# Performance work log

Hardware: AMD Instinct MI355X
Metric: run time of the kernel (lower is better)

The kernel has to match this reference:

```python
import jax, jax.numpy as jnp
import numpy as np

TEMPERATURE = 1.0
NEG_INF = -1e30  # finite stand-in for -inf: safe for log_softmax and its vjp


def setup_inputs() -> dict:
    key = jax.random.key(0)
    k1, k2 = jax.random.split(key)
    B, M, D = 4096, 3, 256
    tokens = jax.random.normal(k1, (B, M, D), dtype=jnp.float32)
    labels = jax.random.randint(k2, (B,), 0, 32, dtype=jnp.int32)
    return {"tokens": tokens, "labels": labels}


def reference(tokens, labels):
    # tokens: [B, M, D]; labels: [B]
    B, M, D = tokens.shape
    # Pairwise per-modality similarities: sim[i, k, m] = <tokens[i,m], tokens[k,m]>
    sim = jnp.einsum('imd,kmd->ikm', tokens, tokens) / TEMPERATURE
    self_mask = jnp.eye(B, dtype=bool)
    # Original excludes sample i itself from the candidate set; masking with a
    # huge negative logit makes it contribute 0 to the softmax partition.
    sim = jnp.where(self_mask[:, :, None], NEG_INF, sim)
    logp = jax.nn.log_softmax(sim, axis=1)  # softmax over the B-1 other samples

    # Positive pairs: same label, excluding self.
    pos = (labels[:, None] == labels[None, :]) & ~self_mask  # [B, B]
    pos_count = pos.sum(axis=1)                               # [B]
    valid = pos_count > 0                                     # sum(same_label) > 1

    # Mean log-prob over positives, per (sample, modality).
    pos_logp = jnp.einsum('ikm,ik->im', logp, pos.astype(logp.dtype))  # [B, M]
    denom = jnp.maximum(pos_count, 1).astype(logp.dtype)[:, None]
    per = jnp.where(valid[:, None], pos_logp / denom, 0.0)             # [B, M]

    num = valid.sum() * M
    return -per.sum() / num.astype(per.dtype)
```

## Files before the change

### kernel.cpp

```cpp
#include <hip/hip_runtime.h>

#define B_N 4096
#define M_N 3
#define D_N 256
#define LOG2E 1.44269504088896340736f
#define LN2   0.69314718055994530942f
#define C_OFF   64.0f
#define T_CLAMP 112.0f

typedef __bf16 bf16x8 __attribute__((ext_vector_type(8)));
typedef float  f32x4  __attribute__((ext_vector_type(4)));

__device__ __forceinline__ unsigned short f2bf(float f) {
    unsigned int u = __float_as_uint(f);
    u += 0x7FFFu + ((u >> 16) & 1u);
    return (unsigned short)(u >> 16);
}
__device__ __forceinline__ float bf2f(unsigned short h) {
    return __uint_as_float(((unsigned int)h) << 16);
}

__global__ void cvt_kernel(const float* __restrict__ in, unsigned short* __restrict__ out,
                           float* __restrict__ norm2) {
    int idx = blockIdx.x * blockDim.x + threadIdx.x;
    float4 v = reinterpret_cast<const float4*>(in)[idx];
    int i   = idx / 192;
    int rem = idx - i * 192;
    int m   = rem >> 6;
    int d4  = rem & 63;
    ushort4 o;
    o.x = f2bf(v.x); o.y = f2bf(v.y); o.z = f2bf(v.z); o.w = f2bf(v.w);
    reinterpret_cast<ushort4*>(out)[((size_t)m * B_N + i) * 64 + d4] = o;
    float nx = bf2f(o.x), ny = bf2f(o.y), nz = bf2f(o.z), nw = bf2f(o.w);
    float s = nx * nx + ny * ny + nz * nz + nw * nw;
#pragma unroll
    for (int msk = 1; msk < 64; msk <<= 1) s += __shfl_xor(s, msk);
    if ((threadIdx.x & 63) == 0) norm2[m * B_N + i] = s;
}

__global__ __launch_bounds__(256, 3) void main_kernel(
    const unsigned short* __restrict__ tokb, const int* __restrict__ labels,
    float2* __restrict__ partials) {
    int raw = blockIdx.x;
    int bid = (raw & 7) * 96 + (raw >> 3);
    int m  = bid >> 8;
    int ns = (bid >> 5) & 7;
    int rb = bid & 31;
    int i0 = rb * 128;
    int cb = ns * 512;

    int tid  = threadIdx.x;
    int wave = tid >> 6, lane = tid & 63;
    int lr = lane & 15, lk = lane >> 4;
    const unsigned short* tm = tokb + (size_t)m * (B_N * D_N);

    __shared__ __align__(16) char ldsB[2][8192];
    __shared__ int labl[512];
    labl[tid]       = labels[cb + tid];
    labl[tid + 256] = labels[cb + tid + 256];

    int r0 = i0 + wave * 32;
    bf16x8 afrag[2][8];
#pragma unroll
    for (int rt = 0; rt < 2; ++rt) {
        const unsigned short* rp = tm + (size_t)(r0 + rt * 16 + lr) * D_N + lk * 8;
#pragma unroll
        for (int kf = 0; kf < 8; ++kf)
            afrag[rt][kf] = *reinterpret_cast<const bf16x8*>(rp + kf * 32);
    }
    int labr[2][4];
#pragma unroll
    for (int rt = 0; rt < 2; ++rt)
#pragma unroll
        for (int j = 0; j < 4; ++j)
            labr[rt][j] = labels[r0 + rt * 16 + lk * 4 + j];

    float S[2][4] = {{0.f, 0.f, 0.f, 0.f}, {0.f, 0.f, 0.f, 0.f}};
    float P[2][4] = {{0.f, 0.f, 0.f, 0.f}, {0.f, 0.f, 0.f, 0.f}};

    int lc  = tid >> 5;
    int w   = tid & 31;
    int sch = w ^ (lc & 7);
    const unsigned short* sbase = tm + (size_t)(cb + lc) * D_N + sch * 8;

    {
        bf16x8 t0 = *reinterpret_cast<const bf16x8*>(sbase);
        bf16x8 t1 = *reinterpret_cast<const bf16x8*>(sbase + 8 * D_N);
        *reinterpret_cast<bf16x8*>(&ldsB[0][tid * 16])        = t0;
        *reinterpret_cast<bf16x8*>(&ldsB[0][4096 + tid * 16]) = t1;
    }

    for (int kb = 0; kb < 32; ++kb) {
        int cur = kb & 1;
        __syncthreads();

        int nkb = (kb + 1) & 31;
        const unsigned short* np = sbase + (size_t)nkb * (16 * D_N);
        bf16x8 nt0 = *reinterpret_cast<const bf16x8*>(np);
        bf16x8 nt1 = *reinterpret_cast<const bf16x8*>(np + 8 * D_N);

        const char* bp = ldsB[cur];
        int swz = (lr & 7) << 4;
        bf16x8 bfrag[8];
#pragma unroll
        for (int kf = 0; kf < 8; ++kf)
            bfrag[kf] = *reinterpret_cast<const bf16x8*>(
                bp + lr * 512 + ((((kf * 4 + lk) << 4)) ^ swz));
        int labc = labl[kb * 16 + lr];

        f32x4 acc0 = {0.f, 0.f, 0.f, 0.f};
        f32x4 acc1 = {0.f, 0.f, 0.f, 0.f};
#pragma unroll
        for (int kf = 0; kf < 8; ++kf) {
            acc0 = __builtin_amdgcn_mfma_f32_16x16x32_bf16(afrag[0][kf], bfrag[kf], acc0, 0, 0, 0);
            acc1 = __builtin_amdgcn_mfma_f32_16x16x32_bf16(afrag[1][kf], bfrag[kf], acc1, 0, 0, 0);
        }

        int cg0 = cb + kb * 16;
        if ((cg0 < r0 + 32) && (cg0 + 16 > r0)) {
            int colg = cg0 + lr;
#pragma unroll
            for (int rt = 0; rt < 2; ++rt) {
                f32x4 aa = rt ? acc1 : acc0;
#pragma unroll
                for (int j = 0; j < 4; ++j) {
                    float s = aa[j];
                    float t = fminf(fmaf(s, LOG2E, -C_OFF), T_CLAMP);
                    float e = __builtin_amdgcn_exp2f(t);
                    int row = r0 + rt * 16 + lk * 4 + j;
                    e = (colg == row) ? 0.f : e;
                    S[rt][j] += e;
                    P[rt][j] += (labc == labr[rt][j]) ? s : 0.f;
                }
            }
        } else {
#pragma unroll
            for (int rt = 0; rt < 2; ++rt) {
                f32x4 aa = rt ? acc1 : acc0;
#pragma unroll
                for (int j = 0; j < 4; ++j) {
                    float s = aa[j];
                    float t = fminf(fmaf(s, LOG2E, -C_OFF), T_CLAMP);
                    S[rt][j] += __builtin_amdgcn_exp2f(t);
                    P[rt][j] += (labc == labr[rt][j]) ? s : 0.f;
                }
            }
        }

        char* dst = (char*)ldsB[cur ^ 1];
        *reinterpret_cast<bf16x8*>(dst + tid * 16)        = nt0;
        *reinterpret_cast<bf16x8*>(dst + 4096 + tid * 16) = nt1;
    }

#pragma unroll
    for (int rt = 0; rt < 2; ++rt)
#pragma unroll
        for (int j = 0; j < 4; ++j) {
            float sv = S[rt][j], pv = P[rt][j];
#pragma unroll
            for (int msk = 1; msk < 16; msk <<= 1) {
                sv += __shfl_xor(sv, msk);
                pv += __shfl_xor(pv, msk);
            }
            if (lr == 0) {
                int rl = rt * 16 + lk * 4 + j;
                float2 q; q.x = sv; q.y = pv;
                partials[(size_t)(((m * 32 + rb) * 8 + ns) * 128) + wave * 32 + rl] = q;
            }
        }
}

__global__ void reduce_kernel(const float2* __restrict__ partials,
                              const float* __restrict__ norm2,
                              const int* __restrict__ labels,
                              float* __restrict__ blockpart,
                              int* __restrict__ nvout) {
    __shared__ int h[32];
    int tid = threadIdx.x;
    if (tid < 32) h[tid] = 0;
    __syncthreads();
    for (int i = tid; i < B_N; i += 256) atomicAdd(&h[labels[i]], 1);
    __syncthreads();
    if (blockIdx.x == 0 && tid == 0) {
        int nv = 0;
#pragma unroll
        for (int c = 0; c < 32; ++c) nv += (h[c] >= 2) ? h[c] : 0;
        nvout[0] = nv;
    }
    int gid = blockIdx.x * 256 + tid;
    int m = gid >> 12, i = gid & 4095;
    int rb = i >> 7, r = i & 127;
    const float2* pp = partials + (size_t)(((m * 32 + rb) * 8) * 128) + r;
    float S = 0.f, P = 0.f;
#pragma unroll
    for (int ns = 0; ns < 8; ++ns) {
        float2 q = pp[ns * 128];
        S += q.x; P += q.y;
    }
    P -= norm2[gid];
    int pc = h[labels[i]] - 1;
    float contrib = (pc > 0)
        ? (__builtin_amdgcn_logf(S) + C_OFF) * LN2 - P / (float)pc
        : 0.f;
#pragma unroll
    for (int off = 32; off >= 1; off >>= 1) contrib += __shfl_down(contrib, off);
    __shared__ float w4[4];
    if ((tid & 63) == 0) w4[tid >> 6] = contrib;
    __syncthreads();
    if (tid == 0) blockpart[blockIdx.x] = w4[0] + w4[1] + w4[2] + w4[3];
}

__global__ void final_kernel(const float* __restrict__ blockpart, const int* __restrict__ nv,
                             float* __restrict__ out) {
    int lane = threadIdx.x;
    float s = (lane < 48) ? blockpart[lane] : 0.f;
#pragma unroll
    for (int off = 32; off >= 1; off >>= 1) s += __shfl_down(s, off);
    if (lane == 0) out[0] = s / (float)(nv[0] * M_N);
}

extern "C" void kernel_launch(void* const* d_in, const int* in_sizes, int n_in,
                              void* d_out, int out_size, void* d_ws, size_t ws_size,
                              hipStream_t stream) {
    const float* tokens = (const float*)d_in[0];
    const int*   labels = (const int*)d_in[1];
    float* out = (float*)d_out;

    char* ws = (char*)d_ws;
    int*    nv        = (int*)(ws + 128);
    float*  blockpart = (float*)(ws + 256);
    float*  norm2     = (float*)(ws + 1024);
    float2* partials  = (float2*)(ws + 65536);
    unsigned short* tokb = (unsigned short*)(ws + 1048576);

    cvt_kernel<<<3072, 256, 0, stream>>>(tokens, tokb, norm2);
    main_kernel<<<768, 256, 0, stream>>>(tokb, labels, partials);
    reduce_kernel<<<48, 256, 0, stream>>>(partials, norm2, labels, blockpart, nv);
    final_kernel<<<1, 64, 0, stream>>>(blockpart, nv, out);
}
```

Measured before the change: 51.25 us.

## Exploit Gram-matrix symmetry by computing only upper-triangular tiles with column sums

The similarity matrix is symmetric, so the main kernel now computes only the upper-triangular 256x256 tile pairs per modality: 136 instead of all pairs. Each off-diagonal tile adds its row-wise exp and positive sums to the row block and also writes column-wise sums, reduced across waves through shared memory, for the mirrored block. This is meant to roughly halve the MFMA and exp work. Per-tile partials are now stored as bf16 and reduced over 16 slots, and occupancy drops to 2 blocks per CU to make room for the larger register tiles. The bf16 partial sums lower the accuracy of the final loss.

```diff
diff --git a/kernel.cpp b/kernel.cpp
--- a/kernel.cpp
+++ b/kernel.cpp
@@ -38,16 +38,18 @@
     if ((threadIdx.x & 63) == 0) norm2[m * B_N + i] = s;
 }
 
-__global__ __launch_bounds__(256, 3) void main_kernel(
+__global__ __launch_bounds__(256, 2) void main_kernel(
     const unsigned short* __restrict__ tokb, const int* __restrict__ labels,
-    float2* __restrict__ partials) {
+    unsigned short* __restrict__ partials) {
     int raw = blockIdx.x;
-    int bid = (raw & 7) * 96 + (raw >> 3);
-    int m  = bid >> 8;
-    int ns = (bid >> 5) & 7;
-    int rb = bid & 31;
-    int i0 = rb * 128;
-    int cb = ns * 512;
+    int bid = (raw & 7) * 51 + (raw >> 3);
+    int m    = bid / 136;
+    int beta = bid - m * 136;
+    int b = 0;
+    while ((b + 1) * (b + 2) / 2 <= beta) ++b;
+    int a = beta - (b * (b + 1)) / 2;
+    bool offd = (a != b);
+    int cb = b * 256;
 
     int tid  = threadIdx.x;
     int wave = tid >> 6, lane = tid & 63;
@@ -55,28 +57,31 @@
     const unsigned short* tm = tokb + (size_t)m * (B_N * D_N);
 
     __shared__ __align__(16) char ldsB[2][8192];
-    __shared__ int labl[512];
-    labl[tid]       = labels[cb + tid];
-    labl[tid + 256] = labels[cb + tid + 256];
-
-    int r0 = i0 + wave * 32;
-    bf16x8 afrag[2][8];
-#pragma unroll
-    for (int rt = 0; rt < 2; ++rt) {
+    __shared__ int labl[256];
+    __shared__ float colbuf[4][16][16][2];
+    labl[tid] = labels[cb + tid];
+
+    int r0 = a * 256 + wave * 64;
+    bf16x8 afrag[4][8];
+#pragma unroll
+    for (int rt = 0; rt < 4; ++rt) {
         const unsigned short* rp = tm + (size_t)(r0 + rt * 16 + lr) * D_N + lk * 8;
 #pragma unroll
         for (int kf = 0; kf < 8; ++kf)
             afrag[rt][kf] = *reinterpret_cast<const bf16x8*>(rp + kf * 32);
     }
-    int labr[2][4];
-#pragma unroll
-    for (int rt = 0; rt < 2; ++rt)
+    int labr[4][4];
+#pragma unroll
+    for (int rt = 0; rt < 4; ++rt)
 #pragma unroll
         for (int j = 0; j < 4; ++j)
             labr[rt][j] = labels[r0 + rt * 16 + lk * 4 + j];
 
-    float S[2][4] = {{0.f, 0.f, 0.f, 0.f}, {0.f, 0.f, 0.f, 0.f}};
-    float P[2][4] = {{0.f, 0.f, 0.f, 0.f}, {0.f, 0.f, 0.f, 0.f}};
+    float S[4][4], P[4][4];
+#pragma unroll
+    for (int rt = 0; rt < 4; ++rt)
+#pragma unroll
+        for (int j = 0; j < 4; ++j) { S[rt][j] = 0.f; P[rt][j] = 0.f; }
 
     int lc  = tid >> 5;
     int w   = tid & 31;
@@ -90,11 +95,11 @@
         *reinterpret_cast<bf16x8*>(&ldsB[0][4096 + tid * 16]) = t1;
     }
 
-    for (int kb = 0; kb < 32; ++kb) {
+    for (int kb = 0; kb < 16; ++kb) {
         int cur = kb & 1;
         __syncthreads();
 
-        int nkb = (kb + 1) & 31;
+        int nkb = (kb + 1) & 15;
         const unsigned short* np = sbase + (size_t)nkb * (16 * D_N);
         bf16x8 nt0 = *reinterpret_cast<const bf16x8*>(np);
         bf16x8 nt1 = *reinterpret_cast<const bf16x8*>(np + 8 * D_N);
@@ -105,55 +110,66 @@
 #pragma unroll
         for (int kf = 0; kf < 8; ++kf)
             bfrag[kf] = *reinterpret_cast<const bf16x8*>(
-                bp + lr * 512 + ((((kf * 4 + lk) << 4)) ^ swz));
+                bp + lr * 512 + (((kf * 4 + lk) << 4) ^ swz));
         int labc = labl[kb * 16 + lr];
 
-        f32x4 acc0 = {0.f, 0.f, 0.f, 0.f};
-        f32x4 acc1 = {0.f, 0.f, 0.f, 0.f};
+        f32x4 acc[4];
+#pragma unroll
+        for (int rt = 0; rt < 4; ++rt) acc[rt] = f32x4{0.f, 0.f, 0.f, 0.f};
 #pragma unroll
         for (int kf = 0; kf < 8; ++kf) {
-            acc0 = __builtin_amdgcn_mfma_f32_16x16x32_bf16(afrag[0][kf], bfrag[kf], acc0, 0, 0, 0);
-            acc1 = __builtin_amdgcn_mfma_f32_16x16x32_bf16(afrag[1][kf], bfrag[kf], acc1, 0, 0, 0);
+#pragma unroll
+            for (int rt = 0; rt < 4; ++rt)
+                acc[rt] = __builtin_amdgcn_mfma_f32_16x16x32_bf16(
+                    afrag[rt][kf], bfrag[kf], acc[rt], 0, 0, 0);
         }
 
+        float cs = 0.f, cp = 0.f;
         int cg0 = cb + kb * 16;
-        if ((cg0 < r0 + 32) && (cg0 + 16 > r0)) {
+        if ((cg0 < r0 + 64) && (cg0 + 16 > r0)) {
             int colg = cg0 + lr;
 #pragma unroll
-            for (int rt = 0; rt < 2; ++rt) {
-                f32x4 aa = rt ? acc1 : acc0;
+            for (int rt = 0; rt < 4; ++rt) {
 #pragma unroll
                 for (int j = 0; j < 4; ++j) {
-                    float s = aa[j];
-                    float t = fminf(fmaf(s, LOG2E, -C_OFF), T_CLAMP);
+                    float s2 = acc[rt][j];
+                    float t = fminf(fmaf(s2, LOG2E, -C_OFF), T_CLAMP);
                     float e = __builtin_amdgcn_exp2f(t);
                     int row = r0 + rt * 16 + lk * 4 + j;
                     e = (colg == row) ? 0.f : e;
-                    S[rt][j] += e;
-                    P[rt][j] += (labc == labr[rt][j]) ? s : 0.f;
+                    bool mt = (labc == labr[rt][j]);
+                    S[rt][j] += e;  P[rt][j] += mt ? s2 : 0.f;
+                    cs += e;        cp += mt ? s2 : 0.f;
                 }
             }
         } else {
 #pragma unroll
-            for (int rt = 0; rt < 2; ++rt) {
-                f32x4 aa = rt ? acc1 : acc0;
+            for (int rt = 0; rt < 4; ++rt) {
 #pragma unroll
                 for (int j = 0; j < 4; ++j) {
-                    float s = aa[j];
-                    float t = fminf(fmaf(s, LOG2E, -C_OFF), T_CLAMP);
-                    S[rt][j] += __builtin_amdgcn_exp2f(t);
-                    P[rt][j] += (labc == labr[rt][j]) ? s : 0.f;
+                    float s2 = acc[rt][j];
+                    float t = fminf(fmaf(s2, LOG2E, -C_OFF), T_CLAMP);
+                    float e = __builtin_amdgcn_exp2f(t);
+                    bool mt = (labc == labr[rt][j]);
+                    S[rt][j] += e;  P[rt][j] += mt ? s2 : 0.f;
+                    cs += e;        cp += mt ? s2 : 0.f;
                 }
             }
         }
+
+        cs += __shfl_xor(cs, 16); cs += __shfl_xor(cs, 32);
+        cp += __shfl_xor(cp, 16); cp += __shfl_xor(cp, 32);
+        if (lk == 0) { colbuf[wave][kb][lr][0] = cs; colbuf[wave][kb][lr][1] = cp; }
 
         char* dst = (char*)ldsB[cur ^ 1];
         *reinterpret_cast<bf16x8*>(dst + tid * 16)        = nt0;
         *reinterpret_cast<bf16x8*>(dst + 4096 + tid * 16) = nt1;
     }
 
-#pragma unroll
-    for (int rt = 0; rt < 2; ++rt)
+    __syncthreads();
+
+#pragma unroll
+    for (int rt = 0; rt < 4; ++rt)
 #pragma unroll
         for (int j = 0; j < 4; ++j) {
             float sv = S[rt][j], pv = P[rt][j];
@@ -163,14 +179,27 @@
                 pv += __shfl_xor(pv, msk);
             }
             if (lr == 0) {
-                int rl = rt * 16 + lk * 4 + j;
-                float2 q; q.x = sv; q.y = pv;
-                partials[(size_t)(((m * 32 + rb) * 8 + ns) * 128) + wave * 32 + rl] = q;
+                int row = r0 + rt * 16 + lk * 4 + j;
+                ushort2 q; q.x = f2bf(sv); q.y = f2bf(pv);
+                *reinterpret_cast<ushort2*>(
+                    partials + ((size_t)(m * B_N + row) * 16 + b) * 2) = q;
             }
         }
-}
-
-__global__ void reduce_kernel(const float2* __restrict__ partials,
+
+    if (offd) {
+        int kb = tid >> 4, cr = tid & 15;
+        float sv = colbuf[0][kb][cr][0] + colbuf[1][kb][cr][0]
+                 + colbuf[2][kb][cr][0] + colbuf[3][kb][cr][0];
+        float pv = colbuf[0][kb][cr][1] + colbuf[1][kb][cr][1]
+                 + colbuf[2][kb][cr][1] + colbuf[3][kb][cr][1];
+        int col = cb + tid;
+        ushort2 q; q.x = f2bf(sv); q.y = f2bf(pv);
+        *reinterpret_cast<ushort2*>(
+            partials + ((size_t)(m * B_N + col) * 16 + a) * 2) = q;
+    }
+}
+
+__global__ void reduce_kernel(const unsigned short* __restrict__ partials,
                               const float* __restrict__ norm2,
                               const int* __restrict__ labels,
                               float* __restrict__ blockpart,
@@ -188,14 +217,13 @@
         nvout[0] = nv;
     }
     int gid = blockIdx.x * 256 + tid;
-    int m = gid >> 12, i = gid & 4095;
-    int rb = i >> 7, r = i & 127;
-    const float2* pp = partials + (size_t)(((m * 32 + rb) * 8) * 128) + r;
+    int i = gid & 4095;
+    const ushort2* pp = reinterpret_cast<const ushort2*>(partials + (size_t)gid * 32);
     float S = 0.f, P = 0.f;
 #pragma unroll
-    for (int ns = 0; ns < 8; ++ns) {
-        float2 q = pp[ns * 128];
-        S += q.x; P += q.y;
+    for (int s = 0; s < 16; ++s) {
+        ushort2 q = pp[s];
+        S += bf2f(q.x); P += bf2f(q.y);
     }
     P -= norm2[gid];
     int pc = h[labels[i]] - 1;
@@ -230,11 +258,11 @@
     int*    nv        = (int*)(ws + 128);
     float*  blockpart = (float*)(ws + 256);
     float*  norm2     = (float*)(ws + 1024);
-    float2* partials  = (float2*)(ws + 65536);
+    unsigned short* partials = (unsigned short*)(ws + 65536);
     unsigned short* tokb = (unsigned short*)(ws + 1048576);
 
     cvt_kernel<<<3072, 256, 0, stream>>>(tokens, tokb, norm2);
-    main_kernel<<<768, 256, 0, stream>>>(tokb, labels, partials);
+    main_kernel<<<408, 256, 0, stream>>>(tokb, labels, partials);
     reduce_kernel<<<48, 256, 0, stream>>>(partials, norm2, labels, blockpart, nv);
     final_kernel<<<1, 64, 0, stream>>>(blockpart, nv, out);
 }
```

New measurement: 98.19 us. 1.92x slower.

## Exploit symmetry of Gram matrix: compute only upper-triangular tiles

Applied to the files above, without the earlier changes.

Gives each block a 128x128 tile on or above the diagonal of the symmetric similarity matrix, so only 528 of 1024 tiles per modality are computed. Off-diagonal tiles add their exp-sums and positive-sums to the row partials and also to the column partials, collected through a new shared buffer and written to the mirrored slot. This roughly halves the MFMA and exp work, at the cost of extra shuffles and LDS traffic, a larger partials buffer, and a reduce step that now reads 32 partials per row. The tile index is recovered with a short serial loop in each block.

```diff
diff --git a/kernel.cpp b/kernel.cpp
--- a/kernel.cpp
+++ b/kernel.cpp
@@ -42,12 +42,14 @@
     const unsigned short* __restrict__ tokb, const int* __restrict__ labels,
     float2* __restrict__ partials) {
     int raw = blockIdx.x;
-    int bid = (raw & 7) * 96 + (raw >> 3);
-    int m  = bid >> 8;
-    int ns = (bid >> 5) & 7;
-    int rb = bid & 31;
-    int i0 = rb * 128;
-    int cb = ns * 512;
+    int bid = (raw & 7) * 198 + (raw >> 3);
+    int m    = bid / 528;
+    int beta = bid - m * 528;
+    int b = 0;
+    while ((b + 1) * (b + 2) / 2 <= beta) ++b;
+    int a = beta - (b * (b + 1)) / 2;
+    bool offd = (a != b);
+    int cb = b * 128;
 
     int tid  = threadIdx.x;
     int wave = tid >> 6, lane = tid & 63;
@@ -55,11 +57,11 @@
     const unsigned short* tm = tokb + (size_t)m * (B_N * D_N);
 
     __shared__ __align__(16) char ldsB[2][8192];
-    __shared__ int labl[512];
-    labl[tid]       = labels[cb + tid];
-    labl[tid + 256] = labels[cb + tid + 256];
-
-    int r0 = i0 + wave * 32;
+    __shared__ int labl[128];
+    __shared__ float colbuf[4][8][16][2];
+    if (tid < 128) labl[tid] = labels[cb + tid];
+
+    int r0 = a * 128 + wave * 32;
     bf16x8 afrag[2][8];
 #pragma unroll
     for (int rt = 0; rt < 2; ++rt) {
@@ -90,11 +92,11 @@
         *reinterpret_cast<bf16x8*>(&ldsB[0][4096 + tid * 16]) = t1;
     }
 
-    for (int kb = 0; kb < 32; ++kb) {
+    for (int kb = 0; kb < 8; ++kb) {
         int cur = kb & 1;
         __syncthreads();
 
-        int nkb = (kb + 1) & 31;
+        int nkb = (kb + 1) & 7;
         const unsigned short* np = sbase + (size_t)nkb * (16 * D_N);
         bf16x8 nt0 = *reinterpret_cast<const bf16x8*>(np);
         bf16x8 nt1 = *reinterpret_cast<const bf16x8*>(np + 8 * D_N);
@@ -105,7 +107,7 @@
 #pragma unroll
         for (int kf = 0; kf < 8; ++kf)
             bfrag[kf] = *reinterpret_cast<const bf16x8*>(
-                bp + lr * 512 + ((((kf * 4 + lk) << 4)) ^ swz));
+                bp + lr * 512 + (((kf * 4 + lk) << 4) ^ swz));
         int labc = labl[kb * 16 + lr];
 
         f32x4 acc0 = {0.f, 0.f, 0.f, 0.f};
@@ -116,6 +118,7 @@
             acc1 = __builtin_amdgcn_mfma_f32_16x16x32_bf16(afrag[1][kf], bfrag[kf], acc1, 0, 0, 0);
         }
 
+        float cs = 0.f, cp = 0.f;
         int cg0 = cb + kb * 16;
         if ((cg0 < r0 + 32) && (cg0 + 16 > r0)) {
             int colg = cg0 + lr;
@@ -124,13 +127,14 @@
                 f32x4 aa = rt ? acc1 : acc0;
 #pragma unroll
                 for (int j = 0; j < 4; ++j) {
-                    float s = aa[j];
-                    float t = fminf(fmaf(s, LOG2E, -C_OFF), T_CLAMP);
+                    float s2 = aa[j];
+                    float t = fminf(fmaf(s2, LOG2E, -C_OFF), T_CLAMP);
                     float e = __builtin_amdgcn_exp2f(t);
                     int row = r0 + rt * 16 + lk * 4 + j;
                     e = (colg == row) ? 0.f : e;
-                    S[rt][j] += e;
-                    P[rt][j] += (labc == labr[rt][j]) ? s : 0.f;
+                    bool mt = (labc == labr[rt][j]);
+                    S[rt][j] += e;  P[rt][j] += mt ? s2 : 0.f;
+                    cs += e;        cp += mt ? s2 : 0.f;
                 }
             }
         } else {
@@ -139,19 +143,27 @@
                 f32x4 aa = rt ? acc1 : acc0;
 #pragma unroll
                 for (int j = 0; j < 4; ++j) {
-                    float s = aa[j];
-                    float t = fminf(fmaf(s, LOG2E, -C_OFF), T_CLAMP);
-                    S[rt][j] += __builtin_amdgcn_exp2f(t);
-                    P[rt][j] += (labc == labr[rt][j]) ? s : 0.f;
+                    float s2 = aa[j];
+                    float t = fminf(fmaf(s2, LOG2E, -C_OFF), T_CLAMP);
+                    float e = __builtin_amdgcn_exp2f(t);
+                    bool mt = (labc == labr[rt][j]);
+                    S[rt][j] += e;  P[rt][j] += mt ? s2 : 0.f;
+                    cs += e;        cp += mt ? s2 : 0.f;
                 }
             }
         }
+
+        cs += __shfl_xor(cs, 16); cs += __shfl_xor(cs, 32);
+        cp += __shfl_xor(cp, 16); cp += __shfl_xor(cp, 32);
+        if (lk == 0) { colbuf[wave][kb][lr][0] = cs; colbuf[wave][kb][lr][1] = cp; }
 
         char* dst = (char*)ldsB[cur ^ 1];
         *reinterpret_cast<bf16x8*>(dst + tid * 16)        = nt0;
         *reinterpret_cast<bf16x8*>(dst + 4096 + tid * 16) = nt1;
     }
 
+    __syncthreads();
+
 #pragma unroll
     for (int rt = 0; rt < 2; ++rt)
 #pragma unroll
@@ -163,11 +175,22 @@
                 pv += __shfl_xor(pv, msk);
             }
             if (lr == 0) {
-                int rl = rt * 16 + lk * 4 + j;
+                int row = r0 + rt * 16 + lk * 4 + j;
                 float2 q; q.x = sv; q.y = pv;
-                partials[(size_t)(((m * 32 + rb) * 8 + ns) * 128) + wave * 32 + rl] = q;
+                partials[(size_t)(b * 3 + m) * B_N + row] = q;
             }
         }
+
+    if (offd && tid < 128) {
+        int kb = tid >> 4, cr = tid & 15;
+        float sv = colbuf[0][kb][cr][0] + colbuf[1][kb][cr][0]
+                 + colbuf[2][kb][cr][0] + colbuf[3][kb][cr][0];
+        float pv = colbuf[0][kb][cr][1] + colbuf[1][kb][cr][1]
+                 + colbuf[2][kb][cr][1] + colbuf[3][kb][cr][1];
+        int col = cb + tid;
+        float2 q; q.x = sv; q.y = pv;
+        partials[(size_t)(a * 3 + m) * B_N + col] = q;
+    }
 }
 
 __global__ void reduce_kernel(const float2* __restrict__ partials,
@@ -189,12 +212,10 @@
     }
     int gid = blockIdx.x * 256 + tid;
     int m = gid >> 12, i = gid & 4095;
-    int rb = i >> 7, r = i & 127;
-    const float2* pp = partials + (size_t)(((m * 32 + rb) * 8) * 128) + r;
     float S = 0.f, P = 0.f;
 #pragma unroll
-    for (int ns = 0; ns < 8; ++ns) {
-        float2 q = pp[ns * 128];
+    for (int s = 0; s < 32; ++s) {
+        float2 q = partials[(size_t)(s * 3 + m) * B_N + i];
         S += q.x; P += q.y;
     }
     P -= norm2[gid];
@@ -231,10 +252,10 @@
     float*  blockpart = (float*)(ws + 256);
     float*  norm2     = (float*)(ws + 1024);
     float2* partials  = (float2*)(ws + 65536);
-    unsigned short* tokb = (unsigned short*)(ws + 1048576);
+    unsigned short* tokb = (unsigned short*)(ws + 3407872);
 
     cvt_kernel<<<3072, 256, 0, stream>>>(tokens, tokb, norm2);
-    main_kernel<<<768, 256, 0, stream>>>(tokb, labels, partials);
+    main_kernel<<<1584, 256, 0, stream>>>(tokb, labels, partials);
     reduce_kernel<<<48, 256, 0, stream>>>(partials, norm2, labels, blockpart, nv);
     final_kernel<<<1, 64, 0, stream>>>(blockpart, nv, out);
 }
```

New measurement: 51.11 us (median of 2 runs). About the same (-0.3%).
